# Kernel tuning notes

Measured on AMD Instinct MI355X. Metric: run time of the kernel, lower is better.

Reference implementation:

```python
import jax, jax.numpy as jnp
import numpy as np

B, T, H, NH = 2, 2048, 2048, 16
HD = H // NH  # 128


def setup_inputs() -> dict:
    key = jax.random.key(0)
    ks = jax.random.split(key, 7)
    s = 1.0 / np.sqrt(H)
    return {
        "x": jax.random.normal(ks[0], (B, T, H), jnp.float32),
        "cos": jax.random.uniform(ks[1], (1, 1, T, HD), jnp.float32),
        "sin": jax.random.uniform(ks[2], (1, 1, T, HD), jnp.float32),
        "Wq": jax.random.normal(ks[3], (H, H), jnp.float32) * s,
        "Wk": jax.random.normal(ks[4], (H, H), jnp.float32) * s,
        "Wv": jax.random.normal(ks[5], (H, H), jnp.float32) * s,
        "Wo": jax.random.normal(ks[6], (H, H), jnp.float32) * s,
    }


def rotate_half(x):
    d = x.shape[-1] // 2
    return jnp.concatenate([-x[..., d:], x[..., :d]], axis=-1)


def reference(x, cos, sin, Wq, Wk, Wv, Wo):
    b, t, h = x.shape
    # torch Linear: y = x @ W.T; reshape to (B, NH, T, HD)
    def proj(W):
        return jnp.einsum('bth,oh->bto', x, W).reshape(b, t, NH, HD).transpose(0, 2, 1, 3)
    q, k, v = proj(Wq), proj(Wk), proj(Wv)
    q = q * cos + rotate_half(q) * sin
    k = k * cos + rotate_half(k) * sin
    scale = 1.0 / jnp.sqrt(jnp.asarray(HD, x.dtype))
    scores = jnp.einsum('bhqd,bhkd->bhqk', q, k) * scale  # [B,NH,T,T]
    causal = jnp.tril(jnp.ones((t, t), bool))
    scores = jnp.where(causal, scores, jnp.asarray(-jnp.inf, scores.dtype))
    attn = jax.nn.softmax(scores, axis=-1)
    out = jnp.einsum('bhqk,bhkd->bhqd', attn, v)  # [B,NH,T,HD]
    out = out.transpose(0, 2, 1, 3).reshape(b, t, h)
    return jnp.einsum('bth,oh->bto', out, Wo)
```

## Files before the change

kernel.cpp:

```cpp
#include <hip/hip_runtime.h>
#include <hip/hip_bf16.h>

#define B_  2
#define T_  2048
#define H_  2048
#define NH_ 16
#define HD_ 128

typedef __attribute__((ext_vector_type(8))) short  short8;
typedef __attribute__((ext_vector_type(4))) float  floatx4;

__device__ __forceinline__ unsigned short f2bf(float x) {
    union { float f; unsigned int u; } c; c.f = x;
    unsigned int r = c.u + 0x7FFF + ((c.u >> 16) & 1);
    return (unsigned short)(r >> 16);
}
__device__ __forceinline__ float bf2f(unsigned short u) {
    union { float f; unsigned int i; } c;
    c.i = ((unsigned int)u) << 16;
    return c.f;
}

__device__ __forceinline__ void gload_lds16(const void* g, void* l) {
    __builtin_amdgcn_global_load_lds(
        (__attribute__((address_space(1))) void*)g,
        (__attribute__((address_space(3))) void*)l, 16, 0, 0);
}

__global__ __launch_bounds__(256) void f32_to_bf16(
    const float* __restrict__ src, unsigned short* __restrict__ dst, int n)
{
    const int i = (blockIdx.x * 256 + threadIdx.x) * 4;
    if (i < n) {
        float4 v = *(const float4*)(src + i);
        ushort4 o;
        o.x = f2bf(v.x); o.y = f2bf(v.y); o.z = f2bf(v.z); o.w = f2bf(v.w);
        *(ushort4*)(dst + i) = o;
    }
}

template<bool BF16_OUT>
__global__ __launch_bounds__(256) void gemm_mfma(
    const unsigned short* __restrict__ A,
    const unsigned short* __restrict__ W,
    float* __restrict__ Yf, unsigned short* __restrict__ Yb,
    int M, int N, int K)
{
    __shared__ __attribute__((aligned(16))) unsigned short Ah[128 * 32];
    __shared__ __attribute__((aligned(16))) unsigned short Bh[128 * 32];

    const int tid  = threadIdx.x;
    const int lane = tid & 63;
    const int n16  = lane & 15;
    const int quad = lane >> 4;
    const int w    = tid >> 6;
    const int wm   = w & 1, wn = w >> 1;

    const int m0 = blockIdx.y * 128;
    const int n0 = blockIdx.x * 128;

    const int srow = tid >> 2;
    const int scol = (tid & 3) * 8;

    floatx4 acc[4][4];
    #pragma unroll
    for (int i = 0; i < 4; i++)
        #pragma unroll
        for (int j = 0; j < 4; j++) acc[i][j] = (floatx4){0.f, 0.f, 0.f, 0.f};

    for (int k0 = 0; k0 < K; k0 += 32) {
        __syncthreads();
        gload_lds16(A + (size_t)(m0 +      srow) * K + k0 + scol, Ah + (size_t)tid * 8);
        gload_lds16(A + (size_t)(m0 + 64 + srow) * K + k0 + scol, Ah + (size_t)(tid + 256) * 8);
        gload_lds16(W + (size_t)(n0 +      srow) * K + k0 + scol, Bh + (size_t)tid * 8);
        gload_lds16(W + (size_t)(n0 + 64 + srow) * K + k0 + scol, Bh + (size_t)(tid + 256) * 8);
        __syncthreads();

        short8 af[4], bfr[4];
        #pragma unroll
        for (int i = 0; i < 4; i++) {
            af[i]  = *(const short8*)(Ah + (wm * 64 + i * 16 + n16) * 32 + quad * 8);
            bfr[i] = *(const short8*)(Bh + (wn * 64 + i * 16 + n16) * 32 + quad * 8);
        }
        #pragma unroll
        for (int i = 0; i < 4; i++)
            #pragma unroll
            for (int j = 0; j < 4; j++)
                acc[i][j] = __builtin_amdgcn_mfma_f32_16x16x32_bf16(af[i], bfr[j], acc[i][j], 0, 0, 0);
    }

    #pragma unroll
    for (int i = 0; i < 4; i++) {
        const int rbase = m0 + wm * 64 + i * 16 + quad * 4;
        #pragma unroll
        for (int r = 0; r < 4; r++) {
            const size_t row = rbase + r;
            #pragma unroll
            for (int j = 0; j < 4; j++) {
                const size_t col = n0 + wn * 64 + j * 16 + n16;
                if (BF16_OUT) Yb[row * N + col] = f2bf(acc[i][j][r]);
                else          Yf[row * N + col] = acc[i][j][r];
            }
        }
    }
}

__global__ __launch_bounds__(256) void rope_convert_qk(
    const unsigned short* __restrict__ qp, const unsigned short* __restrict__ kp,
    const float* __restrict__ cosp, const float* __restrict__ sinp,
    unsigned short* __restrict__ qh, unsigned short* __restrict__ kh)
{
    const int idx  = blockIdx.x * 256 + threadIdx.x;
    const int d    = idx & 63;
    const int rest = idx >> 6;
    const int h    = rest & 15;
    const int bt   = rest >> 4;
    const int t    = bt & (T_ - 1);
    const int b    = bt >> 11;
    const size_t ibase = (size_t)bt * H_ + h * HD_;
    const size_t obase = (((size_t)b * NH_ + h) * T_ + t) * HD_;

    const float c0 = cosp[t*HD_ + d],      s0 = sinp[t*HD_ + d];
    const float c1 = cosp[t*HD_ + d + 64], s1 = sinp[t*HD_ + d + 64];
    const float sc = 0.08838834764831845f;

    float q0 = bf2f(qp[ibase + d]), q1 = bf2f(qp[ibase + d + 64]);
    qh[obase + d]      = f2bf((q0*c0 - q1*s0) * sc);
    qh[obase + d + 64] = f2bf((q1*c1 + q0*s1) * sc);

    float k0 = bf2f(kp[ibase + d]), k1 = bf2f(kp[ibase + d + 64]);
    kh[obase + d]      = f2bf(k0*c0 - k1*s0);
    kh[obase + d + 64] = f2bf(k1*c1 + k0*s1);
}

__global__ __launch_bounds__(256) void transpose_v(
    const unsigned short* __restrict__ vb, unsigned short* __restrict__ vh)
{
    __shared__ float tile[64][65];
    const int t0 = blockIdx.x * 64;
    const int d0 = blockIdx.y * 64;
    const int bh = blockIdx.z;
    const int b  = bh >> 4, h = bh & 15;

    for (int i = threadIdx.x; i < 4096; i += 256) {
        int r = i >> 6, c = i & 63;
        tile[r][c] = bf2f(vb[((size_t)b*T_ + t0 + r) * H_ + h*HD_ + d0 + c]);
    }
    __syncthreads();
    for (int i = threadIdx.x; i < 4096; i += 256) {
        int dr = i >> 6, tc = i & 63;
        vh[((size_t)bh * HD_ + d0 + dr) * T_ + t0 + tc] = f2bf(tile[tc][dr]);
    }
}

__global__ __launch_bounds__(256, 4) void attn_mfma(
    const unsigned short* __restrict__ qh,
    const unsigned short* __restrict__ kh,
    const unsigned short* __restrict__ vh,
    unsigned short* __restrict__ o)
{
    __shared__ __attribute__((aligned(16))) unsigned short Ks[64 * 128];
    __shared__ __attribute__((aligned(16))) unsigned short Vs[128 * 64];
    __shared__ __attribute__((aligned(16))) unsigned short Ps[4][16 * 64];

    const int tid  = threadIdx.x;
    const int lane = tid & 63;
    const int w    = tid >> 6;
    const int n16  = lane & 15;
    const int quad = lane >> 4;

    const int id   = blockIdx.y * gridDim.x + blockIdx.x;
    const int bh   = id & 31;
    const int a    = (id >> 5) & 7;
    const int u    = id >> 8;
    const int qblk = (u < 2) ? (a + (u << 3)) : ((23 + ((u & 1) << 3)) - a);

    const int q0w  = qblk * 64 + w * 16;

    short8 qf[4];
    {
        const size_t qbase = ((size_t)bh * T_ + q0w + n16) * HD_ + quad * 8;
        #pragma unroll
        for (int c = 0; c < 4; c++)
            qf[c] = *(const short8*)(qh + qbase + c * 32);
    }

    const int rk   = tid >> 4;
    const int gk16 = ((tid & 15) ^ (rk & 7)) * 8;
    const unsigned short* ksrc = kh + (size_t)bh * T_ * HD_ + (size_t)rk * HD_ + gk16;
    const int dv   = tid >> 3;
    const int gv16 = ((tid & 7) ^ (dv & 7)) * 8;
    const unsigned short* vsrc = vh + (size_t)bh * HD_ * T_ + (size_t)dv * T_ + gv16;

    floatx4 of[8];
    #pragma unroll
    for (int i = 0; i < 8; i++) of[i] = (floatx4){0.f, 0.f, 0.f, 0.f};
    float mrow[4], lrow[4];
    #pragma unroll
    for (int r = 0; r < 4; r++) { mrow[r] = -INFINITY; lrow[r] = 0.f; }

    const int nkv = qblk + 1;
    for (int kv = 0; kv < nkv; kv++) {
        const int kv0 = kv * 64;
        __syncthreads();
        #pragma unroll
        for (int it = 0; it < 4; it++)
            gload_lds16(ksrc + (size_t)(kv0 + it * 16) * HD_,
                        Ks + (size_t)(it * 256 + tid) * 8);
        #pragma unroll
        for (int it = 0; it < 4; it++)
            gload_lds16(vsrc + kv0 + (size_t)(it * 32) * T_,
                        Vs + (size_t)(it * 256 + tid) * 8);
        __syncthreads();

        floatx4 s[4];
        #pragma unroll
        for (int kg = 0; kg < 4; kg++) {
            floatx4 acc = {0.f, 0.f, 0.f, 0.f};
            #pragma unroll
            for (int c = 0; c < 4; c++) {
                short8 kf = *(const short8*)(Ks + (kg*16 + n16) * 128
                                                + (((c*4 + quad) ^ (n16 & 7)) * 8));
                acc = __builtin_amdgcn_mfma_f32_16x16x32_bf16(qf[c], kf, acc, 0, 0, 0);
            }
            s[kg] = acc;
        }

        const bool needmask = (kv0 + 63 > q0w);

        float alpha[4];
        #pragma unroll
        for (int r = 0; r < 4; r++) {
            const int qrow = q0w + quad * 4 + r;
            float v0 = s[0][r], v1 = s[1][r], v2 = s[2][r], v3 = s[3][r];
            if (needmask) {
                if (kv0 +  0 + n16 > qrow) v0 = -INFINITY;
                if (kv0 + 16 + n16 > qrow) v1 = -INFINITY;
                if (kv0 + 32 + n16 > qrow) v2 = -INFINITY;
                if (kv0 + 48 + n16 > qrow) v3 = -INFINITY;
            }

            float tm = fmaxf(fmaxf(v0, v1), fmaxf(v2, v3));
            tm = fmaxf(tm, __shfl_xor(tm, 1));
            tm = fmaxf(tm, __shfl_xor(tm, 2));
            tm = fmaxf(tm, __shfl_xor(tm, 4));
            tm = fmaxf(tm, __shfl_xor(tm, 8));

            const float mnew = fmaxf(mrow[r], tm);
            const float aa   = __expf(mrow[r] - mnew);
            const float p0 = __expf(v0 - mnew), p1 = __expf(v1 - mnew);
            const float p2 = __expf(v2 - mnew), p3 = __expf(v3 - mnew);

            float ts = p0 + p1 + p2 + p3;
            ts += __shfl_xor(ts, 1);
            ts += __shfl_xor(ts, 2);
            ts += __shfl_xor(ts, 4);
            ts += __shfl_xor(ts, 8);

            lrow[r] = lrow[r] * aa + ts;
            mrow[r] = mnew;
            alpha[r] = aa;

            const int pr = quad * 4 + r;
            const int sx = pr & 7;
            unsigned short* pp = &Ps[w][pr * 64];
            const int g0 = n16 >> 3, e = n16 & 7;
            pp[((g0    ) ^ sx) * 8 + e] = f2bf(p0);
            pp[((g0 + 2) ^ sx) * 8 + e] = f2bf(p1);
            pp[((g0 + 4) ^ sx) * 8 + e] = f2bf(p2);
            pp[((g0 + 6) ^ sx) * 8 + e] = f2bf(p3);
        }
        #pragma unroll
        for (int nt = 0; nt < 8; nt++)
            #pragma unroll
            for (int r = 0; r < 4; r++) of[nt][r] *= alpha[r];

        short8 pf0 = *(const short8*)(&Ps[w][n16 * 64 + ((quad       ^ (n16 & 7)) * 8)]);
        short8 pf1 = *(const short8*)(&Ps[w][n16 * 64 + (((quad + 4) ^ (n16 & 7)) * 8)]);
        #pragma unroll
        for (int nt = 0; nt < 8; nt++) {
            const int vr = (nt * 16 + n16) * 64;
            short8 vf0 = *(const short8*)(Vs + vr + ((quad       ^ (n16 & 7)) * 8));
            short8 vf1 = *(const short8*)(Vs + vr + (((quad + 4) ^ (n16 & 7)) * 8));
            of[nt] = __builtin_amdgcn_mfma_f32_16x16x32_bf16(pf0, vf0, of[nt], 0, 0, 0);
            of[nt] = __builtin_amdgcn_mfma_f32_16x16x32_bf16(pf1, vf1, of[nt], 0, 0, 0);
        }
    }

    const int b = bh >> 4, h = bh & 15;
    #pragma unroll
    for (int r = 0; r < 4; r++) {
        const float inv = 1.f / lrow[r];
        const size_t orow = ((size_t)b * T_ + q0w + quad*4 + r) * H_ + h * HD_;
        #pragma unroll
        for (int nt = 0; nt < 8; nt++)
            o[orow + nt*16 + n16] = f2bf(of[nt][r] * inv);
    }
}

extern "C" void kernel_launch(void* const* d_in, const int* in_sizes, int n_in,
                              void* d_out, int out_size, void* d_ws, size_t ws_size,
                              hipStream_t stream)
{
    const float* x    = (const float*)d_in[0];
    const float* cosp = (const float*)d_in[1];
    const float* sinp = (const float*)d_in[2];
    const float* Wq   = (const float*)d_in[3];
    const float* Wk   = (const float*)d_in[4];
    const float* Wv   = (const float*)d_in[5];
    const float* Wo   = (const float*)d_in[6];

    const size_t NEL  = (size_t)B_ * T_ * H_;
    const size_t NB   = NEL * 4;
    const int    XN   = (int)NEL;
    const int    WN   = H_ * H_;
    char* ws = (char*)d_ws;

    unsigned short* xh   = (unsigned short*)(ws);
    unsigned short* Woh  = (unsigned short*)(ws + NB/2);
    unsigned short* Wqh  = (unsigned short*)(ws + 3*NB/4);
    unsigned short* Wkh  = (unsigned short*)(ws + NB);
    unsigned short* Wvh  = (unsigned short*)(ws + 5*NB/4);
    unsigned short* qpre = (unsigned short*)(ws + 3*NB/2);
    unsigned short* kpre = (unsigned short*)(ws + 2*NB);
    unsigned short* vpre = (unsigned short*)(ws + 5*NB/2);
    unsigned short* qh   = (unsigned short*)(ws + 3*NB);
    unsigned short* kh   = (unsigned short*)(ws + 7*NB/2);
    unsigned short* vh   = (unsigned short*)(ws);
    unsigned short* abh  = (unsigned short*)(ws + 3*NB/2);

    f32_to_bf16<<<XN/1024, 256, 0, stream>>>(x,  xh,  XN);
    f32_to_bf16<<<WN/1024, 256, 0, stream>>>(Wq, Wqh, WN);
    f32_to_bf16<<<WN/1024, 256, 0, stream>>>(Wk, Wkh, WN);
    f32_to_bf16<<<WN/1024, 256, 0, stream>>>(Wv, Wvh, WN);
    f32_to_bf16<<<WN/1024, 256, 0, stream>>>(Wo, Woh, WN);

    const int M = B_ * T_, N = H_, K = H_;
    dim3 gg(N / 128, M / 128);

    gemm_mfma<true><<<gg, 256, 0, stream>>>(xh, Wqh, nullptr, qpre, M, N, K);
    gemm_mfma<true><<<gg, 256, 0, stream>>>(xh, Wkh, nullptr, kpre, M, N, K);
    gemm_mfma<true><<<gg, 256, 0, stream>>>(xh, Wvh, nullptr, vpre, M, N, K);

    rope_convert_qk<<<(B_*T_*NH_*64)/256, 256, 0, stream>>>(qpre, kpre, cosp, sinp, qh, kh);
    transpose_v<<<dim3(T_/64, HD_/64, B_*NH_), 256, 0, stream>>>(vpre, vh);

    attn_mfma<<<dim3(T_/64, B_*NH_), 256, 0, stream>>>(qh, kh, vh, abh);

    gemm_mfma<false><<<gg, 256, 0, stream>>>(abh, Woh, (float*)d_out, nullptr, M, N, K);
}
```

Measured before the change: 487.7 us.

## Fuse QKV projections into one GEMM with double-buffered 256x256 MFMA tiles

```diff
diff --git a/kernel.cpp b/kernel.cpp
--- a/kernel.cpp
+++ b/kernel.cpp
@@ -6,6 +6,7 @@
 #define H_  2048
 #define NH_ 16
 #define HD_ 128
+#define QKVN 6144
 
 typedef __attribute__((ext_vector_type(8))) short  short8;
 typedef __attribute__((ext_vector_type(4))) float  floatx4;
@@ -40,73 +41,139 @@
 }
 
 template<bool BF16_OUT>
-__global__ __launch_bounds__(256) void gemm_mfma(
+__global__ __launch_bounds__(512, 1) void gemm8(
     const unsigned short* __restrict__ A,
     const unsigned short* __restrict__ W,
     float* __restrict__ Yf, unsigned short* __restrict__ Yb,
     int M, int N, int K)
 {
-    __shared__ __attribute__((aligned(16))) unsigned short Ah[128 * 32];
-    __shared__ __attribute__((aligned(16))) unsigned short Bh[128 * 32];
+    __shared__ __attribute__((aligned(16))) unsigned short As[2][256 * 64];
+    __shared__ __attribute__((aligned(16))) unsigned short Bs[2][256 * 64];
 
     const int tid  = threadIdx.x;
     const int lane = tid & 63;
     const int n16  = lane & 15;
     const int quad = lane >> 4;
     const int w    = tid >> 6;
-    const int wm   = w & 1, wn = w >> 1;
-
-    const int m0 = blockIdx.y * 128;
-    const int n0 = blockIdx.x * 128;
-
-    const int srow = tid >> 2;
-    const int scol = (tid & 3) * 8;
-
-    floatx4 acc[4][4];
+    const int wm   = w >> 2;
+    const int wn   = w & 3;
+
+    const int m0 = blockIdx.y * 256;
+    const int n0 = blockIdx.x * 256;
+
+    const int r0  = tid >> 3;
+    const int g0  = ((tid & 7) ^ (r0 & 7)) * 8;
+    const int r1  = r0 + 64;
+    const int g1  = ((tid & 7) ^ (r1 & 7)) * 8;
+    const unsigned short* A0p = A + (size_t)(m0 + r0) * K + g0;
+    const unsigned short* A1p = A + (size_t)(m0 + r1) * K + g1;
+    const unsigned short* B0p = W + (size_t)(n0 + r0) * K + g0;
+    const unsigned short* B1p = W + (size_t)(n0 + r1) * K + g1;
+    const size_t hstep = (size_t)128 * K;
+
+    floatx4 acc[8][4];
     #pragma unroll
-    for (int i = 0; i < 4; i++)
+    for (int i = 0; i < 8; i++)
         #pragma unroll
         for (int j = 0; j < 4; j++) acc[i][j] = (floatx4){0.f, 0.f, 0.f, 0.f};
 
-    for (int k0 = 0; k0 < K; k0 += 32) {
-        __syncthreads();
-        gload_lds16(A + (size_t)(m0 +      srow) * K + k0 + scol, Ah + (size_t)tid * 8);
-        gload_lds16(A + (size_t)(m0 + 64 + srow) * K + k0 + scol, Ah + (size_t)(tid + 256) * 8);
-        gload_lds16(W + (size_t)(n0 +      srow) * K + k0 + scol, Bh + (size_t)tid * 8);
-        gload_lds16(W + (size_t)(n0 + 64 + srow) * K + k0 + scol, Bh + (size_t)(tid + 256) * 8);
-        __syncthreads();
-
-        short8 af[4], bfr[4];
-        #pragma unroll
-        for (int i = 0; i < 4; i++) {
-            af[i]  = *(const short8*)(Ah + (wm * 64 + i * 16 + n16) * 32 + quad * 8);
-            bfr[i] = *(const short8*)(Bh + (wn * 64 + i * 16 + n16) * 32 + quad * 8);
+    const int nt = K >> 6;
+
+    gload_lds16(A0p,         &As[0][(size_t)tid * 8]);
+    gload_lds16(A1p,         &As[0][(size_t)(tid + 512) * 8]);
+    gload_lds16(A0p + hstep, &As[0][8192 + (size_t)tid * 8]);
+    gload_lds16(A1p + hstep, &As[0][8192 + (size_t)(tid + 512) * 8]);
+    gload_lds16(B0p,         &Bs[0][(size_t)tid * 8]);
+    gload_lds16(B1p,         &Bs[0][(size_t)(tid + 512) * 8]);
+    gload_lds16(B0p + hstep, &Bs[0][8192 + (size_t)tid * 8]);
+    gload_lds16(B1p + hstep, &Bs[0][8192 + (size_t)(tid + 512) * 8]);
+
+    for (int t = 0; t < nt; ++t) {
+        const unsigned short* Ac = &As[t & 1][0];
+        const unsigned short* Bc = &Bs[t & 1][0];
+        unsigned short* An = &As[(t & 1) ^ 1][0];
+        unsigned short* Bn = &Bs[(t & 1) ^ 1][0];
+        const bool pre = (t + 1 < nt);
+        const size_t knext = (size_t)(t + 1) << 6;
+
+        short8 bfr[4][2];
+
+        #pragma unroll
+        for (int q = 0; q < 4; ++q) {
+            short8 af[2][2];
+            if (q == 0) {
+                if (pre) {
+                    gload_lds16(A0p + knext,         An + (size_t)tid * 8);
+                    gload_lds16(A1p + knext,         An + (size_t)(tid + 512) * 8);
+                    gload_lds16(A0p + knext + hstep, An + 8192 + (size_t)tid * 8);
+                    gload_lds16(A1p + knext + hstep, An + 8192 + (size_t)(tid + 512) * 8);
+                    asm volatile("s_waitcnt vmcnt(4)" ::: "memory");
+                } else {
+                    asm volatile("s_waitcnt vmcnt(0)" ::: "memory");
+                }
+                asm volatile("s_barrier" ::: "memory");
+                #pragma unroll
+                for (int j = 0; j < 2; ++j)
+                    #pragma unroll
+                    for (int ks = 0; ks < 2; ++ks)
+                        af[j][ks] = *(const short8*)(Ac + (wm*128 + (q*2 + j)*16 + n16) * 64
+                                                        + (((ks*4 + quad) ^ (n16 & 7)) * 8));
+                #pragma unroll
+                for (int ni = 0; ni < 4; ++ni)
+                    #pragma unroll
+                    for (int ks = 0; ks < 2; ++ks)
+                        bfr[ni][ks] = *(const short8*)(Bc + (wn*64 + ni*16 + n16) * 64
+                                                          + (((ks*4 + quad) ^ (n16 & 7)) * 8));
+            } else {
+                #pragma unroll
+                for (int j = 0; j < 2; ++j)
+                    #pragma unroll
+                    for (int ks = 0; ks < 2; ++ks)
+                        af[j][ks] = *(const short8*)(Ac + (wm*128 + (q*2 + j)*16 + n16) * 64
+                                                        + (((ks*4 + quad) ^ (n16 & 7)) * 8));
+                if (q == 1 && pre) {
+                    gload_lds16(B0p + knext,         Bn + (size_t)tid * 8);
+                    gload_lds16(B1p + knext,         Bn + (size_t)(tid + 512) * 8);
+                    gload_lds16(B0p + knext + hstep, Bn + 8192 + (size_t)tid * 8);
+                    gload_lds16(B1p + knext + hstep, Bn + 8192 + (size_t)(tid + 512) * 8);
+                }
+                asm volatile("s_barrier" ::: "memory");
+            }
+            asm volatile("s_waitcnt lgkmcnt(0)" ::: "memory");
+            __builtin_amdgcn_sched_barrier(0);
+            __builtin_amdgcn_s_setprio(1);
+            #pragma unroll
+            for (int ni = 0; ni < 4; ++ni)
+                #pragma unroll
+                for (int ks = 0; ks < 2; ++ks) {
+                    acc[q*2+0][ni] = __builtin_amdgcn_mfma_f32_16x16x32_bf16(
+                        af[0][ks], bfr[ni][ks], acc[q*2+0][ni], 0, 0, 0);
+                    acc[q*2+1][ni] = __builtin_amdgcn_mfma_f32_16x16x32_bf16(
+                        af[1][ks], bfr[ni][ks], acc[q*2+1][ni], 0, 0, 0);
+                }
+            __builtin_amdgcn_s_setprio(0);
+            asm volatile("s_barrier" ::: "memory");
         }
-        #pragma unroll
-        for (int i = 0; i < 4; i++)
+    }
+
+    #pragma unroll
+    for (int mi = 0; mi < 8; ++mi) {
+        const size_t rb = (size_t)(m0 + wm*128 + mi*16 + quad*4);
+        #pragma unroll
+        for (int r = 0; r < 4; ++r) {
+            const size_t row = rb + r;
             #pragma unroll
-            for (int j = 0; j < 4; j++)
-                acc[i][j] = __builtin_amdgcn_mfma_f32_16x16x32_bf16(af[i], bfr[j], acc[i][j], 0, 0, 0);
-    }
-
-    #pragma unroll
-    for (int i = 0; i < 4; i++) {
-        const int rbase = m0 + wm * 64 + i * 16 + quad * 4;
-        #pragma unroll
-        for (int r = 0; r < 4; r++) {
-            const size_t row = rbase + r;
-            #pragma unroll
-            for (int j = 0; j < 4; j++) {
-                const size_t col = n0 + wn * 64 + j * 16 + n16;
-                if (BF16_OUT) Yb[row * N + col] = f2bf(acc[i][j][r]);
-                else          Yf[row * N + col] = acc[i][j][r];
+            for (int ni = 0; ni < 4; ++ni) {
+                const size_t col = n0 + wn*64 + ni*16 + n16;
+                if (BF16_OUT) Yb[row * N + col] = f2bf(acc[mi][ni][r]);
+                else          Yf[row * N + col] = acc[mi][ni][r];
             }
         }
     }
 }
 
 __global__ __launch_bounds__(256) void rope_convert_qk(
-    const unsigned short* __restrict__ qp, const unsigned short* __restrict__ kp,
+    const unsigned short* __restrict__ qkvp,
     const float* __restrict__ cosp, const float* __restrict__ sinp,
     unsigned short* __restrict__ qh, unsigned short* __restrict__ kh)
 {
@@ -117,24 +184,24 @@
     const int bt   = rest >> 4;
     const int t    = bt & (T_ - 1);
     const int b    = bt >> 11;
-    const size_t ibase = (size_t)bt * H_ + h * HD_;
+    const size_t ibase = (size_t)bt * QKVN + h * HD_;
     const size_t obase = (((size_t)b * NH_ + h) * T_ + t) * HD_;
 
     const float c0 = cosp[t*HD_ + d],      s0 = sinp[t*HD_ + d];
     const float c1 = cosp[t*HD_ + d + 64], s1 = sinp[t*HD_ + d + 64];
     const float sc = 0.08838834764831845f;
 
-    float q0 = bf2f(qp[ibase + d]), q1 = bf2f(qp[ibase + d + 64]);
+    float q0 = bf2f(qkvp[ibase + d]), q1 = bf2f(qkvp[ibase + d + 64]);
     qh[obase + d]      = f2bf((q0*c0 - q1*s0) * sc);
     qh[obase + d + 64] = f2bf((q1*c1 + q0*s1) * sc);
 
-    float k0 = bf2f(kp[ibase + d]), k1 = bf2f(kp[ibase + d + 64]);
+    float k0 = bf2f(qkvp[ibase + 2048 + d]), k1 = bf2f(qkvp[ibase + 2048 + d + 64]);
     kh[obase + d]      = f2bf(k0*c0 - k1*s0);
     kh[obase + d + 64] = f2bf(k1*c1 + k0*s1);
 }
 
 __global__ __launch_bounds__(256) void transpose_v(
-    const unsigned short* __restrict__ vb, unsigned short* __restrict__ vh)
+    const unsigned short* __restrict__ qkvp, unsigned short* __restrict__ vh)
 {
     __shared__ float tile[64][65];
     const int t0 = blockIdx.x * 64;
@@ -144,7 +211,7 @@
 
     for (int i = threadIdx.x; i < 4096; i += 256) {
         int r = i >> 6, c = i & 63;
-        tile[r][c] = bf2f(vb[((size_t)b*T_ + t0 + r) * H_ + h*HD_ + d0 + c]);
+        tile[r][c] = bf2f(qkvp[((size_t)b*T_ + t0 + r) * QKVN + 4096 + h*HD_ + d0 + c]);
     }
     __syncthreads();
     for (int i = threadIdx.x; i < 4096; i += 256) {
@@ -264,11 +331,11 @@
             const int pr = quad * 4 + r;
             const int sx = pr & 7;
             unsigned short* pp = &Ps[w][pr * 64];
-            const int g0 = n16 >> 3, e = n16 & 7;
-            pp[((g0    ) ^ sx) * 8 + e] = f2bf(p0);
-            pp[((g0 + 2) ^ sx) * 8 + e] = f2bf(p1);
-            pp[((g0 + 4) ^ sx) * 8 + e] = f2bf(p2);
-            pp[((g0 + 6) ^ sx) * 8 + e] = f2bf(p3);
+            const int g0p = n16 >> 3, e = n16 & 7;
+            pp[((g0p    ) ^ sx) * 8 + e] = f2bf(p0);
+            pp[((g0p + 2) ^ sx) * 8 + e] = f2bf(p1);
+            pp[((g0p + 4) ^ sx) * 8 + e] = f2bf(p2);
+            pp[((g0p + 6) ^ sx) * 8 + e] = f2bf(p3);
         }
         #pragma unroll
         for (int nt = 0; nt < 8; nt++)
@@ -311,41 +378,34 @@
     const float* Wo   = (const float*)d_in[6];
 
     const size_t NEL  = (size_t)B_ * T_ * H_;
-    const size_t NB   = NEL * 4;
     const int    XN   = (int)NEL;
     const int    WN   = H_ * H_;
     char* ws = (char*)d_ws;
-
-    unsigned short* xh   = (unsigned short*)(ws);
-    unsigned short* Woh  = (unsigned short*)(ws + NB/2);
-    unsigned short* Wqh  = (unsigned short*)(ws + 3*NB/4);
-    unsigned short* Wkh  = (unsigned short*)(ws + NB);
-    unsigned short* Wvh  = (unsigned short*)(ws + 5*NB/4);
-    unsigned short* qpre = (unsigned short*)(ws + 3*NB/2);
-    unsigned short* kpre = (unsigned short*)(ws + 2*NB);
-    unsigned short* vpre = (unsigned short*)(ws + 5*NB/2);
-    unsigned short* qh   = (unsigned short*)(ws + 3*NB);
-    unsigned short* kh   = (unsigned short*)(ws + 7*NB/2);
-    unsigned short* vh   = (unsigned short*)(ws);
-    unsigned short* abh  = (unsigned short*)(ws + 3*NB/2);
+    const size_t MB16 = 16777216;
+
+    unsigned short* xh    = (unsigned short*)(ws);
+    unsigned short* Wqkvh = (unsigned short*)(ws + MB16);
+    unsigned short* Woh   = (unsigned short*)(ws + MB16*5/2);
+    unsigned short* qkvp  = (unsigned short*)(ws + 3*MB16);
+    unsigned short* kh    = (unsigned short*)(ws + 6*MB16);
+    unsigned short* qh    = (unsigned short*)(ws + MB16);
+    unsigned short* vh    = (unsigned short*)(ws);
+    unsigned short* abh   = (unsigned short*)(ws + 3*MB16);
 
     f32_to_bf16<<<XN/1024, 256, 0, stream>>>(x,  xh,  XN);
-    f32_to_bf16<<<WN/1024, 256, 0, stream>>>(Wq, Wqh, WN);
-    f32_to_bf16<<<WN/1024, 256, 0, stream>>>(Wk, Wkh, WN);
-    f32_to_bf16<<<WN/1024, 256, 0, stream>>>(Wv, Wvh, WN);
-    f32_to_bf16<<<WN/1024, 256, 0, stream>>>(Wo, Woh, WN);
-
-    const int M = B_ * T_, N = H_, K = H_;
-    dim3 gg(N / 128, M / 128);
-
-    gemm_mfma<true><<<gg, 256, 0, stream>>>(xh, Wqh, nullptr, qpre, M, N, K);
-    gemm_mfma<true><<<gg, 256, 0, stream>>>(xh, Wkh, nullptr, kpre, M, N, K);
-    gemm_mfma<true><<<gg, 256, 0, stream>>>(xh, Wvh, nullptr, vpre, M, N, K);
-
-    rope_convert_qk<<<(B_*T_*NH_*64)/256, 256, 0, stream>>>(qpre, kpre, cosp, sinp, qh, kh);
-    transpose_v<<<dim3(T_/64, HD_/64, B_*NH_), 256, 0, stream>>>(vpre, vh);
+    f32_to_bf16<<<WN/1024, 256, 0, stream>>>(Wq, Wqkvh,          WN);
+    f32_to_bf16<<<WN/1024, 256, 0, stream>>>(Wk, Wqkvh +   WN,   WN);
+    f32_to_bf16<<<WN/1024, 256, 0, stream>>>(Wv, Wqkvh + 2*WN,   WN);
+    f32_to_bf16<<<WN/1024, 256, 0, stream>>>(Wo, Woh,            WN);
+
+    const int M = B_ * T_;
+
+    gemm8<true><<<dim3(QKVN/256, M/256), 512, 0, stream>>>(xh, Wqkvh, nullptr, qkvp, M, QKVN, H_);
+
+    rope_convert_qk<<<(B_*T_*NH_*64)/256, 256, 0, stream>>>(qkvp, cosp, sinp, qh, kh);
+    transpose_v<<<dim3(T_/64, HD_/64, B_*NH_), 256, 0, stream>>>(qkvp, vh);
 
     attn_mfma<<<dim3(T_/64, B_*NH_), 256, 0, stream>>>(qh, kh, vh, abh);
 
-    gemm_mfma<false><<<gg, 256, 0, stream>>>(abh, Woh, (float*)d_out, nullptr, M, N, K);
-}
+    gemm8<false><<<dim3(H_/256, M/256), 512, 0, stream>>>(abh, Woh, (float*)d_out, nullptr, M, H_, H_);
+}
```

After: 489.1 us. About the same (+0.3%).
